# Optimization experiments

Measured on AMD Instinct MI355X. Metric: run time of the kernel, lower is better.

## Reference

```python
import jax, jax.numpy as jnp
import numpy as np

L, B, T, D = 4, 32, 2048, 100


def setup_inputs() -> dict:
    key = jax.random.key(0)
    k1, k2 = jax.random.split(key)
    h = jax.random.normal(k1, (L, B, T, D), dtype=jnp.float32)
    old_h = jax.random.normal(k2, (L, B, T, D), dtype=jnp.float32)
    layer_weights = jnp.ones((L,), dtype=jnp.float32)
    class_weights = jnp.ones((D,), dtype=jnp.float32)
    return {"h": h, "old_h": old_h, "layer_weights": layer_weights, "class_weights": class_weights}


def reference(h, old_h, layer_weights, class_weights):
    # h, old_h: [L, B, T, D]. Softmax / log_softmax are over the T axis
    # (dim=-1 of h[..., c] which is [B, T]).
    logq = jax.nn.log_softmax(h, axis=2)        # student log-probs  [L,B,T,D]
    logp = jax.nn.log_softmax(old_h, axis=2)    # teacher log-probs  [L,B,T,D]
    p = jnp.exp(logp)                            # teacher probs
    # KL(p || q) per (layer, class), batchmean reduction: sum over (B,T) / B
    kl_lc = jnp.sum(p * (logp - logq), axis=(1, 2)) / jnp.float32(B)  # [L, D]
    lw = jax.nn.softmax(layer_weights)           # [L]
    cw = jax.nn.softmax(class_weights)           # [D]
    loss = jnp.einsum('l,ld,d->', lw, kl_lc, cw)
    return loss
```

## Files before the change

kernel.cpp:

```cpp
#include <hip/hip_runtime.h>

constexpr int kL = 4;
constexpr int kB = 32;
constexpr int kT = 2048;
constexpr int kD = 100;
constexpr int kCH = 16;
constexpr int kTSUB = kT / kCH;
constexpr int kROWS = kL * kB * kD;

__global__ __launch_bounds__(256) void kl_partial(
    const float* __restrict__ h, const float* __restrict__ oh,
    float* __restrict__ wsp, float* __restrict__ wsq, float* __restrict__ ww) {
  const int lb = blockIdx.x / kCH;
  const int chunk = blockIdx.x % kCH;
  const int tid = threadIdx.x;
  const int ty = tid >> 6;
  const int dx = tid & 63;
  const int d0 = dx * 2;
  const bool active = (dx < 50);

  const size_t base = ((size_t)lb * kT + (size_t)chunk * kTSUB) * kD;
  const float* __restrict__ hp = h + base;
  const float* __restrict__ op = oh + base;

  float sp0 = 0.f, sp1 = 0.f, sq0 = 0.f, sq1 = 0.f, w0 = 0.f, w1 = 0.f;
  if (active) {
    for (int t = ty; t < kTSUB; t += 4) {
      const size_t off = (size_t)t * kD + d0;
      const float2 hv = *(const float2*)(hp + off);
      const float2 ov = *(const float2*)(op + off);
      const float ep0 = __expf(ov.x), ep1 = __expf(ov.y);
      const float eq0 = __expf(hv.x), eq1 = __expf(hv.y);
      sp0 += ep0; sp1 += ep1;
      sq0 += eq0; sq1 += eq1;
      w0 += ep0 * (ov.x - hv.x);
      w1 += ep1 * (ov.y - hv.y);
    }
  }

  __shared__ float red[256][6];
  red[tid][0] = sp0; red[tid][1] = sp1;
  red[tid][2] = sq0; red[tid][3] = sq1;
  red[tid][4] = w0;  red[tid][5] = w1;
  __syncthreads();
  if (ty == 0 && active) {
    float a0 = 0.f, a1 = 0.f, a2 = 0.f, a3 = 0.f, a4 = 0.f, a5 = 0.f;
    #pragma unroll
    for (int g = 0; g < 4; ++g) {
      const float* r = red[g * 64 + dx];
      a0 += r[0]; a1 += r[1]; a2 += r[2]; a3 += r[3]; a4 += r[4]; a5 += r[5];
    }
    const int r = lb * kD + d0;
    atomicAdd(&wsp[r], a0);     atomicAdd(&wsp[r + 1], a1);
    atomicAdd(&wsq[r], a2);     atomicAdd(&wsq[r + 1], a3);
    atomicAdd(&ww[r], a4);      atomicAdd(&ww[r + 1], a5);
  }
}

__global__ __launch_bounds__(256) void kl_final(
    const float* __restrict__ wsp, const float* __restrict__ wsq,
    const float* __restrict__ ww, const float* __restrict__ lwin,
    const float* __restrict__ cwin, float* __restrict__ out) {
  __shared__ float lw[kL];
  __shared__ float cw[kD];
  __shared__ float red[256];
  const int tid = threadIdx.x;

  if (tid == 0) {
    float m = lwin[0];
    for (int i = 1; i < kL; ++i) m = fmaxf(m, lwin[i]);
    float s = 0.f;
    for (int i = 0; i < kL; ++i) { const float e = __expf(lwin[i] - m); lw[i] = e; s += e; }
    const float inv = 1.0f / s;
    for (int i = 0; i < kL; ++i) lw[i] *= inv;
  }
  if (tid == 64) {
    float m = cwin[0];
    for (int i = 1; i < kD; ++i) m = fmaxf(m, cwin[i]);
    float s = 0.f;
    for (int i = 0; i < kD; ++i) { const float e = __expf(cwin[i] - m); cw[i] = e; s += e; }
    const float inv = 1.0f / s;
    for (int i = 0; i < kD; ++i) cw[i] *= inv;
  }
  __syncthreads();

  float acc = 0.f;
  for (int r = tid; r < kROWS; r += 256) {
    const int l = r / (kB * kD);
    const int d = r % kD;
    const float sp = wsp[r], sq = wsq[r], w = ww[r];
    const float val = w / sp - __logf(sp) + __logf(sq);
    acc += lw[l] * cw[d] * val;
  }
  red[tid] = acc;
  __syncthreads();
  for (int s = 128; s > 0; s >>= 1) {
    if (tid < s) red[tid] += red[tid + s];
    __syncthreads();
  }
  if (tid == 0) out[0] = red[0] / (float)kB;
}

extern "C" void kernel_launch(void* const* d_in, const int* in_sizes, int n_in,
                              void* d_out, int out_size, void* d_ws, size_t ws_size,
                              hipStream_t stream) {
  const float* h    = (const float*)d_in[0];
  const float* oh   = (const float*)d_in[1];
  const float* lwin = (const float*)d_in[2];
  const float* cwin = (const float*)d_in[3];

  float* wsp = (float*)d_ws;
  float* wsq = wsp + kROWS;
  float* ww  = wsq + kROWS;
  hipMemsetAsync(d_ws, 0, (size_t)3 * kROWS * sizeof(float), stream);

  kl_partial<<<kL * kB * kCH, 256, 0, stream>>>(h, oh, wsp, wsq, ww);
  kl_final<<<1, 256, 0, stream>>>(wsp, wsq, ww, lwin, cwin, (float*)d_out);
}
```

Before: 258.0 us.

## Use float4 loads in partial kernel and parallelize final reduction across blocks

The partial kernel now reads float4 vectors, with each wave covering two time rows of 25 float4s, in place of float2 loads with 50 active lanes. This raises bytes per load and lane utilization on the bandwidth-bound pass. The single-block final reduction over 12800 rows becomes a 50-block reduce that atomically accumulates into a scalar, followed by a tiny write kernel. This adds a third kernel launch and a float atomic, which makes the summation order nondeterministic.

```diff
diff --git a/kernel.cpp b/kernel.cpp
--- a/kernel.cpp
+++ b/kernel.cpp
@@ -4,75 +4,89 @@
 constexpr int kB = 32;
 constexpr int kT = 2048;
 constexpr int kD = 100;
+constexpr int kD4 = kD / 4;
 constexpr int kCH = 16;
 constexpr int kTSUB = kT / kCH;
 constexpr int kROWS = kL * kB * kD;
 
 __global__ __launch_bounds__(256) void kl_partial(
-    const float* __restrict__ h, const float* __restrict__ oh,
+    const float4* __restrict__ h4, const float4* __restrict__ oh4,
     float* __restrict__ wsp, float* __restrict__ wsq, float* __restrict__ ww) {
-  const int lb = blockIdx.x / kCH;
-  const int chunk = blockIdx.x % kCH;
+  const int lb = blockIdx.x >> 4;
+  const int chunk = blockIdx.x & 15;
   const int tid = threadIdx.x;
   const int ty = tid >> 6;
-  const int dx = tid & 63;
-  const int d0 = dx * 2;
-  const bool active = (dx < 50);
+  const int lane = tid & 63;
+  const int half = lane / kD4;
+  const int d4 = lane - half * kD4;
+  const bool active = (lane < 2 * kD4);
 
-  const size_t base = ((size_t)lb * kT + (size_t)chunk * kTSUB) * kD;
-  const float* __restrict__ hp = h + base;
-  const float* __restrict__ op = oh + base;
+  float4 sp = {0.f, 0.f, 0.f, 0.f};
+  float4 sq = {0.f, 0.f, 0.f, 0.f};
+  float4 w  = {0.f, 0.f, 0.f, 0.f};
 
-  float sp0 = 0.f, sp1 = 0.f, sq0 = 0.f, sq1 = 0.f, w0 = 0.f, w1 = 0.f;
   if (active) {
-    for (int t = ty; t < kTSUB; t += 4) {
-      const size_t off = (size_t)t * kD + d0;
-      const float2 hv = *(const float2*)(hp + off);
-      const float2 ov = *(const float2*)(op + off);
+    const int row0 = chunk * kTSUB + ty * 2 + half;
+    const size_t b4 = ((size_t)lb * kT + row0) * kD4 + d4;
+    const float4* __restrict__ hp = h4 + b4;
+    const float4* __restrict__ op = oh4 + b4;
+#pragma unroll 4
+    for (int i = 0; i < kTSUB / 8; ++i) {
+      const size_t off = (size_t)i * 8 * kD4;
+      const float4 hv = hp[off];
+      const float4 ov = op[off];
       const float ep0 = __expf(ov.x), ep1 = __expf(ov.y);
-      const float eq0 = __expf(hv.x), eq1 = __expf(hv.y);
-      sp0 += ep0; sp1 += ep1;
-      sq0 += eq0; sq1 += eq1;
-      w0 += ep0 * (ov.x - hv.x);
-      w1 += ep1 * (ov.y - hv.y);
+      const float ep2 = __expf(ov.z), ep3 = __expf(ov.w);
+      sp.x += ep0; sp.y += ep1; sp.z += ep2; sp.w += ep3;
+      sq.x += __expf(hv.x); sq.y += __expf(hv.y);
+      sq.z += __expf(hv.z); sq.w += __expf(hv.w);
+      w.x += ep0 * (ov.x - hv.x); w.y += ep1 * (ov.y - hv.y);
+      w.z += ep2 * (ov.z - hv.z); w.w += ep3 * (ov.w - hv.w);
     }
   }
 
-  __shared__ float red[256][6];
-  red[tid][0] = sp0; red[tid][1] = sp1;
-  red[tid][2] = sq0; red[tid][3] = sq1;
-  red[tid][4] = w0;  red[tid][5] = w1;
+  __shared__ float red[256][12];
+  {
+    float* r = red[tid];
+    r[0] = sp.x; r[1] = sp.y; r[2]  = sp.z; r[3]  = sp.w;
+    r[4] = sq.x; r[5] = sq.y; r[6]  = sq.z; r[7]  = sq.w;
+    r[8] = w.x;  r[9] = w.y;  r[10] = w.z;  r[11] = w.w;
+  }
   __syncthreads();
-  if (ty == 0 && active) {
-    float a0 = 0.f, a1 = 0.f, a2 = 0.f, a3 = 0.f, a4 = 0.f, a5 = 0.f;
-    #pragma unroll
+  if (tid < kD) {
+    const int dd4 = tid >> 2, j = tid & 3;
+    float asp = 0.f, asq = 0.f, aw = 0.f;
+#pragma unroll
     for (int g = 0; g < 4; ++g) {
-      const float* r = red[g * 64 + dx];
-      a0 += r[0]; a1 += r[1]; a2 += r[2]; a3 += r[3]; a4 += r[4]; a5 += r[5];
+#pragma unroll
+      for (int hh = 0; hh < 2; ++hh) {
+        const float* s = red[g * 64 + hh * kD4 + dd4];
+        asp += s[j]; asq += s[4 + j]; aw += s[8 + j];
+      }
     }
-    const int r = lb * kD + d0;
-    atomicAdd(&wsp[r], a0);     atomicAdd(&wsp[r + 1], a1);
-    atomicAdd(&wsq[r], a2);     atomicAdd(&wsq[r + 1], a3);
-    atomicAdd(&ww[r], a4);      atomicAdd(&ww[r + 1], a5);
+    const int idx = lb * kD + tid;
+    atomicAdd(&wsp[idx], asp);
+    atomicAdd(&wsq[idx], asq);
+    atomicAdd(&ww[idx],  aw);
   }
 }
 
-__global__ __launch_bounds__(256) void kl_final(
+__global__ __launch_bounds__(256) void kl_reduce(
     const float* __restrict__ wsp, const float* __restrict__ wsq,
     const float* __restrict__ ww, const float* __restrict__ lwin,
-    const float* __restrict__ cwin, float* __restrict__ out) {
+    const float* __restrict__ cwin, float* __restrict__ acc) {
   __shared__ float lw[kL];
   __shared__ float cw[kD];
-  __shared__ float red[256];
+  __shared__ float sred[256];
   const int tid = threadIdx.x;
 
   if (tid == 0) {
     float m = lwin[0];
     for (int i = 1; i < kL; ++i) m = fmaxf(m, lwin[i]);
-    float s = 0.f;
-    for (int i = 0; i < kL; ++i) { const float e = __expf(lwin[i] - m); lw[i] = e; s += e; }
+    float e[kL], s = 0.f;
+    for (int i = 0; i < kL; ++i) { e[i] = __expf(lwin[i] - m); s += e[i]; }
     const float inv = 1.0f / s;
-    for (int i = 0; i < kL; ++i) lw[i] *= inv;
+    for (int i = 0; i < kL; ++i) lw[i] = e[i] * inv;
   }
   if (tid == 64) {
     float m = cwin[0];
@@ -84,21 +98,22 @@
   }
   __syncthreads();
 
-  float acc = 0.f;
-  for (int r = tid; r < kROWS; r += 256) {
-    const int l = r / (kB * kD);
-    const int d = r % kD;
-    const float sp = wsp[r], sq = wsq[r], w = ww[r];
-    const float val = w / sp - __logf(sp) + __logf(sq);
-    acc += lw[l] * cw[d] * val;
-  }
-  red[tid] = acc;
+  const int r = blockIdx.x * 256 + tid;
+  const int l = r / (kB * kD);
+  const int d = r % kD;
+  const float spv = wsp[r], sqv = wsq[r], wv = ww[r];
+  const float val = wv / spv - __logf(spv) + __logf(sqv);
+  sred[tid] = lw[l] * cw[d] * val;
   __syncthreads();
   for (int s = 128; s > 0; s >>= 1) {
-    if (tid < s) red[tid] += red[tid + s];
+    if (tid < s) sred[tid] += sred[tid + s];
     __syncthreads();
   }
-  if (tid == 0) out[0] = red[0] / (float)kB;
+  if (tid == 0) atomicAdd(acc, sred[0]);
+}
+
+__global__ void kl_write(const float* __restrict__ acc, float* __restrict__ out) {
+  out[0] = acc[0] / (float)kB;
 }
 
 extern "C" void kernel_launch(void* const* d_in, const int* in_sizes, int n_in,
@@ -112,8 +127,11 @@
   float* wsp = (float*)d_ws;
   float* wsq = wsp + kROWS;
   float* ww  = wsq + kROWS;
-  hipMemsetAsync(d_ws, 0, (size_t)3 * kROWS * sizeof(float), stream);
+  float* acc = ww + kROWS;
+  hipMemsetAsync(d_ws, 0, ((size_t)3 * kROWS + 1) * sizeof(float), stream);
 
-  kl_partial<<<kL * kB * kCH, 256, 0, stream>>>(h, oh, wsp, wsq, ww);
-  kl_final<<<1, 256, 0, stream>>>(wsp, wsq, ww, lwin, cwin, (float*)d_out);
+  kl_partial<<<kL * kB * kCH, 256, 0, stream>>>(
+      (const float4*)h, (const float4*)oh, wsp, wsq, ww);
+  kl_reduce<<<kROWS / 256, 256, 0, stream>>>(wsp, wsq, ww, lwin, cwin, acc);
+  kl_write<<<1, 1, 0, stream>>>(acc, (float*)d_out);
 }
```

Result: faster. 243.1 us (-5.8%).
